# Kernel tuning notes

Measured on AMD Instinct MI355X. Metric: run time of the kernel, lower is better.

The kernel has to match this reference:

```python
import jax, jax.numpy as jnp
import numpy as np

B, C, H, W, K = 4, 96, 56, 56, 9
CM = 2 * C  # graph-conv output channels (standard Grapher: 2*in_channels)


def setup_inputs() -> dict:
    key = jax.random.key(0)
    ks = jax.random.split(key, 6)
    x = jax.random.normal(ks[0], (B, C, H, W), jnp.float32)
    fc1_w = jax.random.normal(ks[1], (C, C), jnp.float32) * 0.05
    fc1_b = jnp.zeros((C,), jnp.float32)
    gconv_w = jax.random.normal(ks[2], (CM, 2 * C), jnp.float32) * 0.05
    gconv_b = jnp.zeros((CM,), jnp.float32)
    fc2_w = jax.random.normal(ks[3], (C, CM), jnp.float32) * 0.05
    fc2_b = jnp.zeros((C,), jnp.float32)
    sa_w = jax.random.normal(ks[4], (1, 2, 7, 7), jnp.float32) * 0.05
    return dict(x=x, fc1_w=fc1_w, fc1_b=fc1_b, gconv_w=gconv_w, gconv_b=gconv_b,
                fc2_w=fc2_w, fc2_b=fc2_b, sa_w=sa_w)


def _knn_idx(xf, k):
    # xf: (B, C, N) -> (B, N, k) nearest-neighbor indices (includes self),
    # matching dense_knn_matrix: topk of negative squared euclidean distance.
    x2 = jnp.sum(xf * xf, axis=1)                       # (B, N)
    inner = jnp.einsum('bcn,bcm->bnm', xf, xf)          # (B, N, N)
    dist = x2[:, :, None] - 2.0 * inner + x2[:, None, :]
    _, idx = jax.lax.top_k(-dist, k)                    # (B, N, k)
    return idx


def _grapher(x, fc1_w, fc1_b, gconv_w, gconv_b, fc2_w, fc2_b, sa_w):
    shortcut = x
    # fc1: 1x1 conv C -> C
    h = jnp.einsum('bchw,oc->bohw', x, fc1_w) + fc1_b[None, :, None, None]
    b, c, hh, ww = h.shape
    n = hh * ww
    xf = h.reshape(b, c, n)                              # nodes: (B, C, N)
    idx = _knn_idx(xf, K)                                # dynamic KNN graph
    # EdgeConv2d: gather x_j at neighbor indices, x_i = center
    xt = jnp.transpose(xf, (0, 2, 1))                    # (B, N, C)
    x_j = jax.vmap(lambda t, i: t[i])(xt, idx)           # (B, N, K, C)
    x_j = jnp.transpose(x_j, (0, 3, 1, 2))               # (B, C, N, K)
    x_i = xf[:, :, :, None]                              # (B, C, N, 1)
    feat = jnp.concatenate(
        [jnp.broadcast_to(x_i, x_j.shape), x_j - x_i], axis=1)  # (B, 2C, N, K)
    e = jnp.einsum('bcnk,oc->bonk', feat, gconv_w) + gconv_b[None, :, None, None]
    e = jax.nn.relu(e)
    g = jnp.max(e, axis=-1)                              # max over K neighbors
    g = g.reshape(b, CM, hh, ww)
    # fc2: 1x1 conv 2C -> C
    out = jnp.einsum('bchw,oc->bohw', g, fc2_w) + fc2_b[None, :, None, None]
    # SpatialAttention: channel mean/max -> 7x7 conv -> sigmoid gate
    avg = jnp.mean(out, axis=1, keepdims=True)
    mx = jnp.max(out, axis=1, keepdims=True)
    sa_in = jnp.concatenate([avg, mx], axis=1)           # (B, 2, H, W)
    att = jax.lax.conv_general_dilated(
        sa_in, sa_w, window_strides=(1, 1), padding=[(3, 3), (3, 3)],
        dimension_numbers=('NCHW', 'OIHW', 'NCHW'))
    att = jax.nn.sigmoid(att)
    return out * att + shortcut


def reference(x, fc1_w, fc1_b, gconv_w, gconv_b, fc2_w, fc2_b, sa_w):
    return _grapher(x, fc1_w, fc1_b, gconv_w, gconv_b, fc2_w, fc2_b, sa_w)
```

## Files before the change

kernel.cpp:

```cpp
#include <hip/hip_runtime.h>

#define BB 4
#define CC 96
#define NN 3136
#define FLTMAX 3.402823466e+38f
#define CAP 44
#define DELTA 1.0f

typedef unsigned short ushort_t;
typedef __attribute__((ext_vector_type(8))) short bf16x8;
typedef __attribute__((ext_vector_type(4))) float f32x4;

__device__ __forceinline__ ushort_t f2bf(float f) {
    unsigned u = __float_as_uint(f);
    unsigned r = (u + 0x7fff + ((u >> 16) & 1)) >> 16;
    return (ushort_t)r;
}
__device__ __forceinline__ float bf2f(ushort_t us) {
    return __uint_as_float(((unsigned)us) << 16);
}


__global__ __launch_bounds__(256) void k_fc1(const float* __restrict__ x, const float* __restrict__ w,
                                             const float* __restrict__ bias, float* __restrict__ h,
                                             float* __restrict__ x2g,
                                             ushort_t* __restrict__ hAhi,
                                             float* __restrict__ hT) {
    __shared__ float sm[96 * 98 + 96 * 64];
    float* wT = sm;
    float* xl = sm + 96 * 98;
    const int tid = threadIdx.x;
    const int n0 = blockIdx.x * 64;
    const int b = blockIdx.y;
    for (int i = tid; i < 96 * 96; i += 256) {
        int o = i / 96, c = i - o * 96;
        wT[c * 98 + o] = w[i];
    }
    const float* xb = x + (size_t)b * CC * NN;
    for (int i = tid; i < 96 * 64; i += 256) {
        int c = i >> 6, nl = i & 63;
        xl[i] = xb[(size_t)c * NN + n0 + nl];
    }
    __syncthreads();
    const int tr = tid >> 4, tc = tid & 15;
    float acc[6][4];
#pragma unroll
    for (int i = 0; i < 6; ++i)
#pragma unroll
        for (int j = 0; j < 4; ++j) acc[i][j] = 0.f;
#pragma unroll 4
    for (int c = 0; c < 96; ++c) {
        float4 xv = *(const float4*)&xl[c * 64 + tc * 4];
        const float* wp = &wT[c * 98 + tr * 6];
        float2 w01 = *(const float2*)(wp);
        float2 w23 = *(const float2*)(wp + 2);
        float2 w45 = *(const float2*)(wp + 4);
        float wv[6] = {w01.x, w01.y, w23.x, w23.y, w45.x, w45.y};
        float xj[4] = {xv.x, xv.y, xv.z, xv.w};
#pragma unroll
        for (int i = 0; i < 6; ++i)
#pragma unroll
            for (int j = 0; j < 4; ++j) acc[i][j] = fmaf(wv[i], xj[j], acc[i][j]);
    }
    float* hb = h + (size_t)b * CC * NN;
    float* hTb = hT + (size_t)b * NN * 96;
    ushort_t* thi = hAhi + (size_t)b * 602112;
#pragma unroll
    for (int i = 0; i < 6; ++i) {
        float bi = bias[tr * 6 + i];
        acc[i][0] += bi; acc[i][1] += bi; acc[i][2] += bi; acc[i][3] += bi;
        float4 o4 = make_float4(acc[i][0], acc[i][1], acc[i][2], acc[i][3]);
        *(float4*)&hb[(size_t)(tr * 6 + i) * NN + n0 + tc * 4] = o4;
        const int c = tr * 6 + i;
        const int cpart = c >> 3;
#pragma unroll
        for (int j = 0; j < 4; ++j) {
            const int n = n0 + tc * 4 + j;
            const int idx = (((n >> 5) * 12 + cpart) * 32 + (n & 31)) * 8 + (c & 7);
            thi[idx] = f2bf(acc[i][j]);
            hTb[(size_t)n * 96 + c] = acc[i][j];
        }
    }
    __syncthreads();
#pragma unroll
    for (int j = 0; j < 4; ++j) {
        float s = 0.f;
#pragma unroll
        for (int i = 0; i < 6; ++i) s = fmaf(acc[i][j], acc[i][j], s);
        sm[tr * 64 + tc * 4 + j] = s;
    }
    __syncthreads();
    if (tid < 64) {
        float s = 0.f;
#pragma unroll
        for (int t = 0; t < 16; ++t) s += sm[t * 64 + tid];
        x2g[(size_t)b * NN + n0 + tid] = s;
    }
}

#define MFMA_TILE_HI(t, acc0, acc1, acc2, acc3)                                       \
    {                                                                                 \
        const int abase_ = (t) * 6144;                                                \
        _Pragma("unroll")                                                             \
        for (int ks_ = 0; ks_ < 3; ++ks_) {                                           \
            const int base_ = abase_ + ks_ * 1024;                                    \
            bf16x8 a0_ = *(const bf16x8*)(hHi + base_ + aoff0);                       \
            bf16x8 a1_ = *(const bf16x8*)(hHi + base_ + aoff1);                       \
            bf16x8 a2_ = *(const bf16x8*)(hHi + base_ + 3072 + aoff0);                \
            bf16x8 a3_ = *(const bf16x8*)(hHi + base_ + 3072 + aoff1);                \
            acc0 = __builtin_amdgcn_mfma_f32_16x16x32_bf16(a0_, bhi[ks_], acc0, 0, 0, 0); \
            acc1 = __builtin_amdgcn_mfma_f32_16x16x32_bf16(a1_, bhi[ks_], acc1, 0, 0, 0); \
            acc2 = __builtin_amdgcn_mfma_f32_16x16x32_bf16(a2_, bhi[ks_], acc2, 0, 0, 0); \
            acc3 = __builtin_amdgcn_mfma_f32_16x16x32_bf16(a3_, bhi[ks_], acc3, 0, 0, 0); \
        }                                                                             \
    }

__global__ __launch_bounds__(256) void k_dist(const ushort_t* __restrict__ hAhi,
                                              const float* __restrict__ x2,
                                              int* __restrict__ cand_cnt,
                                              int* __restrict__ cand_idx) {
    __shared__ float thrb[32][24];
    __shared__ float thr_s[32];
    __shared__ int   cnt[32];
    __shared__ int   list[32][CAP];
    const int tid = threadIdx.x;
    const int nb = blockIdx.x, q = blockIdx.y, b = blockIdx.z;
    const int w = tid >> 6, l = tid & 63;
    const int ln = l & 15, lq = l >> 4;
    const int p = w >> 1;
    const int kl_off = lq * 256;
    const ushort_t* hHi = hAhi + (size_t)b * 602112;
    const float* x2b = x2 + (size_t)b * NN;

    const int lane32n = (w & 1) * 16 + ln;
    bf16x8 bhi[3];
#pragma unroll
    for (int ks = 0; ks < 3; ++ks) {
        const int off = nb * 3072 + ks * 1024 + kl_off + lane32n * 8;
        bhi[ks] = *(const bf16x8*)(hHi + off);
    }
    const int aoff0 = kl_off + ln * 8;
    const int aoff1 = kl_off + (16 + ln) * 8;

    const int qb0 = (q == 0) ? 0 : (q == 1) ? 13 : (q == 2) ? 25 : 37;
    const int qb1 = (q == 0) ? 13 : (q == 1) ? 25 : (q == 2) ? 37 : 49;
    const int tstart = qb0 + p;

    unsigned scache[7][8];
    float lv0 = FLTMAX, lv1 = FLTMAX, lv2 = FLTMAX;
#pragma unroll
    for (int ti = 0; ti < 7; ++ti) {
        const int t = tstart + 2 * ti;
        if (t < qb1) {
            const int m0 = t * 64;
            f32x4 acc0 = {0.f, 0.f, 0.f, 0.f}, acc1 = {0.f, 0.f, 0.f, 0.f};
            f32x4 acc2 = {0.f, 0.f, 0.f, 0.f}, acc3 = {0.f, 0.f, 0.f, 0.f};
            MFMA_TILE_HI(t, acc0, acc1, acc2, acc3);
#pragma unroll
            for (int msub = 0; msub < 4; ++msub) {
                f32x4 a = (msub == 0) ? acc0 : (msub == 1) ? acc1 : (msub == 2) ? acc2 : acc3;
                const int mb = m0 + msub * 16 + lq * 4;
                float4 xv = *(const float4*)&x2b[mb];
                float s0 = fmaf(-2.f, a[0], xv.x);
                float s1 = fmaf(-2.f, a[1], xv.y);
                float s2 = fmaf(-2.f, a[2], xv.z);
                float s3 = fmaf(-2.f, a[3], xv.w);
                scache[ti][msub * 2 + 0] = ((unsigned)f2bf(s0) << 16) | (unsigned)f2bf(s1);
                scache[ti][msub * 2 + 1] = ((unsigned)f2bf(s2) << 16) | (unsigned)f2bf(s3);
                float ss[4] = {s0, s1, s2, s3};
#pragma unroll
                for (int r = 0; r < 4; ++r) {
                    float v = ss[r];
                    float t0 = fminf(lv0, v);
                    lv0 = fmaxf(t0, lv1);
                    float t1 = fminf(t0, lv1);
                    lv1 = fmaxf(t1, lv2);
                    lv2 = fminf(t1, lv2);
                }
            }
        }
    }
    {
        const int sidx = (p * 4 + lq) * 3;
        thrb[lane32n][sidx + 0] = lv0;
        thrb[lane32n][sidx + 1] = lv1;
        thrb[lane32n][sidx + 2] = lv2;
    }
    __syncthreads();
    if (tid < 32) {
        float tmp[24];
#pragma unroll
        for (int j = 0; j < 24; ++j) tmp[j] = thrb[tid][j];
        float last = FLTMAX;
        for (int kk = 0; kk < 9; ++kk) {
            float mn = FLTMAX; int ms = 0;
            for (int j = 0; j < 24; ++j)
                if (tmp[j] < mn) { mn = tmp[j]; ms = j; }
            tmp[ms] = FLTMAX;
            last = mn;
        }
        thr_s[tid] = last + DELTA;
        cnt[tid] = 0;
    }
    __syncthreads();
    const float thr = thr_s[lane32n];

#pragma unroll
    for (int ti = 0; ti < 7; ++ti) {
        const int t = tstart + 2 * ti;
        if (t < qb1) {
            const int m0 = t * 64;
#pragma unroll
            for (int msub = 0; msub < 4; ++msub) {
                const int mb = m0 + msub * 16 + lq * 4;
                const unsigned u01 = scache[ti][msub * 2 + 0];
                const unsigned u23 = scache[ti][msub * 2 + 1];
                float vv[4] = {bf2f((ushort_t)(u01 >> 16)), bf2f((ushort_t)(u01 & 0xffff)),
                               bf2f((ushort_t)(u23 >> 16)), bf2f((ushort_t)(u23 & 0xffff))};
#pragma unroll
                for (int r = 0; r < 4; ++r) {
                    if (vv[r] <= thr) {
                        int pos = atomicAdd(&cnt[lane32n], 1);
                        if (pos < CAP) list[lane32n][pos] = mb + r;
                    }
                }
            }
        }
    }
    __syncthreads();
    const size_t rowbase = (size_t)b * NN + nb * 32;
    if (tid < 32) cand_cnt[(rowbase + tid) * 4 + q] = min(cnt[tid], CAP);
    for (int i = tid; i < 32 * CAP; i += 256) {
        int r = i / CAP, j = i - r * CAP;
        if (j < min(cnt[r], CAP))
            cand_idx[((rowbase + r) * 4 + q) * CAP + j] = list[r][j];
    }
}

__global__ __launch_bounds__(256) void k_merge9(const int* __restrict__ cand_cnt,
                                                const int* __restrict__ cand_idx,
                                                const float* __restrict__ hT,
                                                const float* __restrict__ x2,
                                                int* __restrict__ idx9) {
    const int tid = threadIdx.x;
    const int wv = tid >> 6, lane = tid & 63;
    const size_t n = (size_t)blockIdx.x * 4 + wv;
    const int b = (int)(n / NN);
    const int nn = (int)(n - (size_t)b * NN);
    const int c0 = cand_cnt[n * 4 + 0];
    const int c1 = cand_cnt[n * 4 + 1];
    const int c2 = cand_cnt[n * 4 + 2];
    const int c3 = cand_cnt[n * 4 + 3];
    const int p1 = c0, p2 = c0 + c1, p3 = c0 + c1 + c2;
    const int ct = p3 + c3;
    const float* hTb = hT + (size_t)b * NN * 96;
    const float* own = hTb + (size_t)nn * 96;
    const float* x2b = x2 + (size_t)b * NN;

    float vs[3]; int cjs[3];
#pragma unroll
    for (int t = 0; t < 3; ++t) { vs[t] = FLTMAX; cjs[t] = 0x7fffffff; }
#pragma unroll
    for (int t = 0; t < 3; ++t) {
        const int j = lane + 64 * t;
        if (j < ct) {
            const int qq = (j >= p1) + (j >= p2) + (j >= p3);
            const int base = (qq == 0) ? 0 : (qq == 1) ? p1 : (qq == 2) ? p2 : p3;
            const int cj = cand_idx[(n * 4 + qq) * CAP + (j - base)];
            const float* cr = hTb + (size_t)cj * 96;
            float dot = 0.f;
#pragma unroll
            for (int i = 0; i < 24; ++i) {
                float4 rv = *(const float4*)&own[i * 4];
                float4 cv4 = *(const float4*)&cr[i * 4];
                dot = fmaf(rv.x, cv4.x, dot);
                dot = fmaf(rv.y, cv4.y, dot);
                dot = fmaf(rv.z, cv4.z, dot);
                dot = fmaf(rv.w, cv4.w, dot);
            }
            vs[t] = fmaf(-2.f, dot, x2b[cj]);
            cjs[t] = cj;
        }
    }
    int* dst = idx9 + n * 9;
    for (int kk = 0; kk < 9; ++kk) {
        float mv = vs[0]; int mi = cjs[0];
        if (vs[1] < mv || (vs[1] == mv && cjs[1] < mi)) { mv = vs[1]; mi = cjs[1]; }
        if (vs[2] < mv || (vs[2] == mv && cjs[2] < mi)) { mv = vs[2]; mi = cjs[2]; }
#pragma unroll
        for (int s = 32; s; s >>= 1) {
            float ov = __shfl_xor(mv, s, 64);
            int oi = __shfl_xor(mi, s, 64);
            if (ov < mv || (ov == mv && oi < mi)) { mv = ov; mi = oi; }
        }
        if (lane == 0) dst[kk] = mi;
#pragma unroll
        for (int t = 0; t < 3; ++t)
            if (cjs[t] == mi) vs[t] = FLTMAX;
    }
}

__global__ __launch_bounds__(256) void k_ac(const float* __restrict__ h, const float* __restrict__ gw,
                                            const float* __restrict__ gb, ushort_t* __restrict__ acT) {
    __shared__ float sm[96 * 98 + 96 * 64];
    float* wT = sm;
    float* hl = sm + 96 * 98;
    const int tid = threadIdx.x;
    const int n0 = blockIdx.x * 64, ot = blockIdx.y, b = blockIdx.z;
    for (int i = tid; i < 96 * 96; i += 256) {
        int o = i / 96, c = i - o * 96;
        float v;
        if (ot < 2) {
            const float* gwp = gw + (size_t)(ot * 96 + o) * 192;
            v = gwp[c] - gwp[96 + c];
        } else {
            v = gw[(size_t)((ot - 2) * 96 + o) * 192 + 96 + c];
        }
        wT[c * 98 + o] = v;
    }
    const float* hb = h + (size_t)b * CC * NN;
    for (int i = tid; i < 96 * 64; i += 256) {
        int c = i >> 6, nl = i & 63;
        hl[i] = hb[(size_t)c * NN + n0 + nl];
    }
    __syncthreads();
    const int tr = tid >> 4, tc = tid & 15;
    float acc[6][4];
#pragma unroll
    for (int i = 0; i < 6; ++i)
#pragma unroll
        for (int j = 0; j < 4; ++j) acc[i][j] = 0.f;
#pragma unroll 4
    for (int c = 0; c < 96; ++c) {
        float4 xv = *(const float4*)&hl[c * 64 + tc * 4];
        const float* wp = &wT[c * 98 + tr * 6];
        float2 w01 = *(const float2*)(wp);
        float2 w23 = *(const float2*)(wp + 2);
        float2 w45 = *(const float2*)(wp + 4);
        float wv[6] = {w01.x, w01.y, w23.x, w23.y, w45.x, w45.y};
        float xj[4] = {xv.x, xv.y, xv.z, xv.w};
#pragma unroll
        for (int i = 0; i < 6; ++i)
#pragma unroll
            for (int j = 0; j < 4; ++j) acc[i][j] = fmaf(wv[i], xj[j], acc[i][j]);
    }
    const int obase = ot * 96 + tr * 6;
    float bs[6];
#pragma unroll
    for (int i = 0; i < 6; ++i) bs[i] = (ot < 2) ? gb[obase + i] : 0.f;
#pragma unroll
    for (int j = 0; j < 4; ++j) {
        ushort_t* dst = acT + ((size_t)b * NN + n0 + tc * 4 + j) * 384 + obase;
        ushort2 p0, p1, p2;
        p0.x = f2bf(acc[0][j] + bs[0]); p0.y = f2bf(acc[1][j] + bs[1]);
        p1.x = f2bf(acc[2][j] + bs[2]); p1.y = f2bf(acc[3][j] + bs[3]);
        p2.x = f2bf(acc[4][j] + bs[4]); p2.y = f2bf(acc[5][j] + bs[5]);
        *(ushort2*)(dst + 0) = p0;
        *(ushort2*)(dst + 2) = p1;
        *(ushort2*)(dst + 4) = p2;
    }
}

__global__ __launch_bounds__(256) void k_gather(const ushort_t* __restrict__ acT,
                                                const int* __restrict__ idx9,
                                                float* __restrict__ gT) {
    const int lane = threadIdx.x & 63;
    const int wv = threadIdx.x >> 6;
    const int b = blockIdx.y;
    const int nb = blockIdx.x * 16 + wv * 4;
    for (int r = 0; r < 4; ++r) {
        const int n = nb + r;
        const ushort_t* ar = acT + ((size_t)b * NN + n) * 384;
        float a0 = bf2f(ar[lane]), a1 = bf2f(ar[lane + 64]), a2 = bf2f(ar[lane + 128]);
        const int* ip = idx9 + ((size_t)b * NN + n) * 9;
        int jj[9];
#pragma unroll
        for (int k = 0; k < 9; ++k) jj[k] = ip[k];
        float m0 = -FLTMAX, m1 = -FLTMAX, m2 = -FLTMAX;
#pragma unroll
        for (int k = 0; k < 9; ++k) {
            const ushort_t* cr = acT + ((size_t)b * NN + jj[k]) * 384 + 192;
            m0 = fmaxf(m0, a0 + bf2f(cr[lane]));
            m1 = fmaxf(m1, a1 + bf2f(cr[lane + 64]));
            m2 = fmaxf(m2, a2 + bf2f(cr[lane + 128]));
        }
        float* gr = gT + ((size_t)b * NN + n) * 192;
        gr[lane] = fmaxf(m0, 0.f);
        gr[lane + 64] = fmaxf(m1, 0.f);
        gr[lane + 128] = fmaxf(m2, 0.f);
    }
}

__global__ __launch_bounds__(256) void k_fc2(const float* __restrict__ gT, const float* __restrict__ w,
                                             const float* __restrict__ bias, float* __restrict__ out,
                                             float* __restrict__ sa_in) {
    __shared__ float Wc[96 * 36];
    __shared__ float Gc[64 * 36];
    const int tid = threadIdx.x;
    const int n0 = blockIdx.x * 64, b = blockIdx.y;
    const int tr = tid >> 4, tc = tid & 15;
    float acc[6][4];
#pragma unroll
    for (int i = 0; i < 6; ++i)
#pragma unroll
        for (int j = 0; j < 4; ++j) acc[i][j] = 0.f;
    for (int kc = 0; kc < 192; kc += 32) {
        for (int i = tid; i < 96 * 32; i += 256) {
            int c = i >> 5, k = i & 31;
            Wc[c * 36 + k] = w[(size_t)c * 192 + kc + k];
        }
        for (int i = tid; i < 64 * 32; i += 256) {
            int nl = i >> 5, k = i & 31;
            Gc[nl * 36 + k] = gT[((size_t)b * NN + n0 + nl) * 192 + kc + k];
        }
        __syncthreads();
#pragma unroll
        for (int k = 0; k < 32; k += 4) {
            float4 wv[6]; float4 gv[4];
#pragma unroll
            for (int i = 0; i < 6; ++i) wv[i] = *(const float4*)&Wc[(tr * 6 + i) * 36 + k];
#pragma unroll
            for (int j = 0; j < 4; ++j) gv[j] = *(const float4*)&Gc[(tc * 4 + j) * 36 + k];
#pragma unroll
            for (int i = 0; i < 6; ++i)
#pragma unroll
                for (int j = 0; j < 4; ++j) {
                    acc[i][j] = fmaf(wv[i].x, gv[j].x, acc[i][j]);
                    acc[i][j] = fmaf(wv[i].y, gv[j].y, acc[i][j]);
                    acc[i][j] = fmaf(wv[i].z, gv[j].z, acc[i][j]);
                    acc[i][j] = fmaf(wv[i].w, gv[j].w, acc[i][j]);
                }
        }
        __syncthreads();
    }
    float* ob = out + (size_t)b * CC * NN;
    float bs[6];
#pragma unroll
    for (int i = 0; i < 6; ++i) bs[i] = bias[tr * 6 + i];
    float ps[4], pm[4];
#pragma unroll
    for (int j = 0; j < 4; ++j) { ps[j] = 0.f; pm[j] = -FLTMAX; }
#pragma unroll
    for (int i = 0; i < 6; ++i) {
        float o0 = acc[i][0] + bs[i], o1 = acc[i][1] + bs[i];
        float o2 = acc[i][2] + bs[i], o3 = acc[i][3] + bs[i];
        *(float4*)&ob[(size_t)(tr * 6 + i) * NN + n0 + tc * 4] = make_float4(o0, o1, o2, o3);
        ps[0] += o0; ps[1] += o1; ps[2] += o2; ps[3] += o3;
        pm[0] = fmaxf(pm[0], o0); pm[1] = fmaxf(pm[1], o1);
        pm[2] = fmaxf(pm[2], o2); pm[3] = fmaxf(pm[3], o3);
    }
    float* red  = Wc;
    float* red2 = Wc + 1024;
#pragma unroll
    for (int j = 0; j < 4; ++j) {
        red[tr * 64 + tc * 4 + j]  = ps[j];
        red2[tr * 64 + tc * 4 + j] = pm[j];
    }
    __syncthreads();
    if (tid < 64) {
        float s_ = 0.f, m_ = -FLTMAX;
#pragma unroll
        for (int t = 0; t < 16; ++t) { s_ += red[t * 64 + tid]; m_ = fmaxf(m_, red2[t * 64 + tid]); }
        sa_in[(size_t)b * 2 * NN + n0 + tid] = s_ * (1.0f / 96.0f);
        sa_in[(size_t)b * 2 * NN + NN + n0 + tid] = m_;
    }
}

__global__ __launch_bounds__(256) void k_att(const float* __restrict__ sa_in, const float* __restrict__ sw,
                                             const float* __restrict__ x, float* __restrict__ out) {
    int n = blockIdx.x * 256 + threadIdx.x;
    int b = blockIdx.y;
    if (n >= NN) return;
    int y = n / 56, xw = n - y * 56;
    float acc = 0.f;
#pragma unroll
    for (int ci = 0; ci < 2; ++ci) {
        const float* sb = sa_in + ((size_t)b * 2 + ci) * NN;
#pragma unroll
        for (int dy = 0; dy < 7; ++dy) {
            int yy = y + dy - 3;
            if ((unsigned)yy < 56u) {
#pragma unroll
                for (int dx = 0; dx < 7; ++dx) {
                    int xx = xw + dx - 3;
                    if ((unsigned)xx < 56u)
                        acc = fmaf(sb[yy * 56 + xx], sw[(ci * 7 + dy) * 7 + dx], acc);
                }
            }
        }
    }
    float att = 1.f / (1.f + expf(-acc));
    const float* xb = x + (size_t)b * CC * NN + n;
    float* ob = out + (size_t)b * CC * NN + n;
#pragma unroll 4
    for (int c = 0; c < 96; ++c) {
        size_t o = (size_t)c * NN;
        ob[o] = fmaf(ob[o], att, xb[o]);
    }
}

extern "C" void kernel_launch(void* const* d_in, const int* in_sizes, int n_in,
                              void* d_out, int out_size, void* d_ws, size_t ws_size,
                              hipStream_t stream) {
    (void)in_sizes; (void)n_in; (void)out_size; (void)ws_size;
    const float* x       = (const float*)d_in[0];
    const float* fc1_w   = (const float*)d_in[1];
    const float* fc1_b   = (const float*)d_in[2];
    const float* gconv_w = (const float*)d_in[3];
    const float* gconv_b = (const float*)d_in[4];
    const float* fc2_w   = (const float*)d_in[5];
    const float* fc2_b   = (const float*)d_in[6];
    const float* sa_w    = (const float*)d_in[7];
    float* out = (float*)d_out;

    float* ws   = (float*)d_ws;
    float* h    = ws;
    float* x2   = h + (size_t)BB * CC * NN;
    int*   idx9 = (int*)(x2 + BB * NN);
    float* regA = (float*)(idx9 + (size_t)BB * NN * 9);
    ushort_t* hAhi = (ushort_t*)regA;
    ushort_t* acT  = (ushort_t*)regA;
    float* hT   = regA + 2408448;
    float* regB = hT + 1204224;
    int*   cand_idx = (int*)regB;
    int*   cand_cnt = (int*)(regB + 2207744);
    float* gT   = regB;
    float* sa_in = regB + 2408448;

    k_fc1   <<<dim3(49, BB), 256, 0, stream>>>(x, fc1_w, fc1_b, h, x2, hAhi, hT);
    k_dist  <<<dim3(98, 4, BB), 256, 0, stream>>>(hAhi, x2, cand_cnt, cand_idx);
    k_merge9<<<dim3(3136), 256, 0, stream>>>(cand_cnt, cand_idx, hT, x2, idx9);
    k_ac    <<<dim3(49, 4, BB), 256, 0, stream>>>(h, gconv_w, gconv_b, acT);
    k_gather<<<dim3(196, BB), 256, 0, stream>>>(acT, idx9, gT);
    k_fc2   <<<dim3(49, BB), 256, 0, stream>>>(gT, fc2_w, fc2_b, out, sa_in);
    k_att   <<<dim3(13, BB), 256, 0, stream>>>(sa_in, sa_w, x, out);
}
```

Before: 269.9 us.

## Prefilter KNN candidates by packed approximate distance; shrink fc2 tile for more blocks

The distance kernel now stores each candidate's bf16 approximate distance in the upper 16 bits of its index word. The merge kernel uses these packed values to find the 9th-smallest approximate distance. It then recomputes exact fp32 dot products only for candidates within a fixed margin of that value, which skips most of the 96-wide gathers. Separately, fc2 drops from a 64-node tile to a 16-node tile with one output column per thread, launching four times as many blocks to fill more CUs, at the cost of reloading the weight tile more often. The margin-based pruning assumes the bf16 error is bounded by the margin and could change the selected neighbours if it is not.

```diff
diff --git a/kernel.cpp b/kernel.cpp
--- a/kernel.cpp
+++ b/kernel.cpp
@@ -6,6 +6,7 @@
 #define FLTMAX 3.402823466e+38f
 #define CAP 44
 #define DELTA 1.0f
+#define PREF_MARGIN 0.8f
 
 typedef unsigned short ushort_t;
 typedef __attribute__((ext_vector_type(8))) short bf16x8;
@@ -215,13 +216,12 @@
                 const int mb = m0 + msub * 16 + lq * 4;
                 const unsigned u01 = scache[ti][msub * 2 + 0];
                 const unsigned u23 = scache[ti][msub * 2 + 1];
-                float vv[4] = {bf2f((ushort_t)(u01 >> 16)), bf2f((ushort_t)(u01 & 0xffff)),
-                               bf2f((ushort_t)(u23 >> 16)), bf2f((ushort_t)(u23 & 0xffff))};
+                unsigned bits[4] = {u01 >> 16, u01 & 0xffffu, u23 >> 16, u23 & 0xffffu};
 #pragma unroll
                 for (int r = 0; r < 4; ++r) {
-                    if (vv[r] <= thr) {
+                    if (bf2f((ushort_t)bits[r]) <= thr) {
                         int pos = atomicAdd(&cnt[lane32n], 1);
-                        if (pos < CAP) list[lane32n][pos] = mb + r;
+                        if (pos < CAP) list[lane32n][pos] = (int)((bits[r] << 16) | (unsigned)(mb + r));
                     }
                 }
             }
@@ -257,16 +257,46 @@
     const float* own = hTb + (size_t)nn * 96;
     const float* x2b = x2 + (size_t)b * NN;
 
-    float vs[3]; int cjs[3];
-#pragma unroll
-    for (int t = 0; t < 3; ++t) { vs[t] = FLTMAX; cjs[t] = 0x7fffffff; }
+    float av[3]; int cjs[3];
+#pragma unroll
+    for (int t = 0; t < 3; ++t) { av[t] = FLTMAX; cjs[t] = 0x7fffffff; }
 #pragma unroll
     for (int t = 0; t < 3; ++t) {
         const int j = lane + 64 * t;
         if (j < ct) {
             const int qq = (j >= p1) + (j >= p2) + (j >= p3);
             const int base = (qq == 0) ? 0 : (qq == 1) ? p1 : (qq == 2) ? p2 : p3;
-            const int cj = cand_idx[(n * 4 + qq) * CAP + (j - base)];
+            const unsigned u = (unsigned)cand_idx[(n * 4 + qq) * CAP + (j - base)];
+            av[t] = bf2f((ushort_t)(u >> 16));
+            cjs[t] = (int)(u & 0xffffu);
+        }
+    }
+    float a9 = FLTMAX;
+    {
+        float tv[3] = {av[0], av[1], av[2]};
+        for (int kk = 0; kk < 9; ++kk) {
+            float mv = tv[0]; int ms = 0;
+            if (tv[1] < mv) { mv = tv[1]; ms = 1; }
+            if (tv[2] < mv) { mv = tv[2]; ms = 2; }
+            int mid = lane * 4 + ms;
+#pragma unroll
+            for (int s = 32; s; s >>= 1) {
+                float ov = __shfl_xor(mv, s, 64);
+                int oi = __shfl_xor(mid, s, 64);
+                if (ov < mv || (ov == mv && oi < mid)) { mv = ov; mid = oi; }
+            }
+            a9 = mv;
+            if ((mid >> 2) == lane) tv[mid & 3] = FLTMAX;
+        }
+    }
+    const float cutoff = a9 + PREF_MARGIN;
+
+    float vs[3];
+#pragma unroll
+    for (int t = 0; t < 3; ++t) {
+        vs[t] = FLTMAX;
+        if (av[t] <= cutoff) {
+            const int cj = cjs[t];
             const float* cr = hTb + (size_t)cj * 96;
             float dot = 0.f;
 #pragma unroll
@@ -279,7 +309,6 @@
                 dot = fmaf(rv.w, cv4.w, dot);
             }
             vs[t] = fmaf(-2.f, dot, x2b[cj]);
-            cjs[t] = cj;
         }
     }
     int* dst = idx9 + n * 9;
@@ -395,72 +424,54 @@
                                              const float* __restrict__ bias, float* __restrict__ out,
                                              float* __restrict__ sa_in) {
     __shared__ float Wc[96 * 36];
-    __shared__ float Gc[64 * 36];
+    __shared__ float Gc[16 * 36];
+    __shared__ float red[2][16][17];
     const int tid = threadIdx.x;
-    const int n0 = blockIdx.x * 64, b = blockIdx.y;
+    const int n0 = blockIdx.x * 16, b = blockIdx.y;
     const int tr = tid >> 4, tc = tid & 15;
-    float acc[6][4];
-#pragma unroll
-    for (int i = 0; i < 6; ++i)
-#pragma unroll
-        for (int j = 0; j < 4; ++j) acc[i][j] = 0.f;
+    float acc[6];
+#pragma unroll
+    for (int i = 0; i < 6; ++i) acc[i] = 0.f;
     for (int kc = 0; kc < 192; kc += 32) {
         for (int i = tid; i < 96 * 32; i += 256) {
             int c = i >> 5, k = i & 31;
             Wc[c * 36 + k] = w[(size_t)c * 192 + kc + k];
         }
-        for (int i = tid; i < 64 * 32; i += 256) {
+        for (int i = tid; i < 16 * 32; i += 256) {
             int nl = i >> 5, k = i & 31;
             Gc[nl * 36 + k] = gT[((size_t)b * NN + n0 + nl) * 192 + kc + k];
         }
         __syncthreads();
 #pragma unroll
         for (int k = 0; k < 32; k += 4) {
-            float4 wv[6]; float4 gv[4];
-#pragma unroll
-            for (int i = 0; i < 6; ++i) wv[i] = *(const float4*)&Wc[(tr * 6 + i) * 36 + k];
-#pragma unroll
-            for (int j = 0; j < 4; ++j) gv[j] = *(const float4*)&Gc[(tc * 4 + j) * 36 + k];
-#pragma unroll
-            for (int i = 0; i < 6; ++i)
-#pragma unroll
-                for (int j = 0; j < 4; ++j) {
-                    acc[i][j] = fmaf(wv[i].x, gv[j].x, acc[i][j]);
-                    acc[i][j] = fmaf(wv[i].y, gv[j].y, acc[i][j]);
-                    acc[i][j] = fmaf(wv[i].z, gv[j].z, acc[i][j]);
-                    acc[i][j] = fmaf(wv[i].w, gv[j].w, acc[i][j]);
-                }
+            float4 gv = *(const float4*)&Gc[tc * 36 + k];
+#pragma unroll
+            for (int i = 0; i < 6; ++i) {
+                float4 wv = *(const float4*)&Wc[(tr * 6 + i) * 36 + k];
+                acc[i] = fmaf(wv.x, gv.x, acc[i]);
+                acc[i] = fmaf(wv.y, gv.y, acc[i]);
+                acc[i] = fmaf(wv.z, gv.z, acc[i]);
+                acc[i] = fmaf(wv.w, gv.w, acc[i]);
+            }
         }
         __syncthreads();
     }
     float* ob = out + (size_t)b * CC * NN;
-    float bs[6];
-#pragma unroll
-    for (int i = 0; i < 6; ++i) bs[i] = bias[tr * 6 + i];
-    float ps[4], pm[4];
-#pragma unroll
-    for (int j = 0; j < 4; ++j) { ps[j] = 0.f; pm[j] = -FLTMAX; }
+    float ps = 0.f, pm = -FLTMAX;
 #pragma unroll
     for (int i = 0; i < 6; ++i) {
-        float o0 = acc[i][0] + bs[i], o1 = acc[i][1] + bs[i];
-        float o2 = acc[i][2] + bs[i], o3 = acc[i][3] + bs[i];
-        *(float4*)&ob[(size_t)(tr * 6 + i) * NN + n0 + tc * 4] = make_float4(o0, o1, o2, o3);
-        ps[0] += o0; ps[1] += o1; ps[2] += o2; ps[3] += o3;
-        pm[0] = fmaxf(pm[0], o0); pm[1] = fmaxf(pm[1], o1);
-        pm[2] = fmaxf(pm[2], o2); pm[3] = fmaxf(pm[3], o3);
-    }
-    float* red  = Wc;
-    float* red2 = Wc + 1024;
-#pragma unroll
-    for (int j = 0; j < 4; ++j) {
-        red[tr * 64 + tc * 4 + j]  = ps[j];
-        red2[tr * 64 + tc * 4 + j] = pm[j];
-    }
-    __syncthreads();
-    if (tid < 64) {
+        float o = acc[i] + bias[tr * 6 + i];
+        ob[(size_t)(tr * 6 + i) * NN + n0 + tc] = o;
+        ps += o;
+        pm = fmaxf(pm, o);
+    }
+    red[0][tr][tc] = ps;
+    red[1][tr][tc] = pm;
+    __syncthreads();
+    if (tid < 16) {
         float s_ = 0.f, m_ = -FLTMAX;
 #pragma unroll
-        for (int t = 0; t < 16; ++t) { s_ += red[t * 64 + tid]; m_ = fmaxf(m_, red2[t * 64 + tid]); }
+        for (int t = 0; t < 16; ++t) { s_ += red[0][t][tid]; m_ = fmaxf(m_, red[1][t][tid]); }
         sa_in[(size_t)b * 2 * NN + n0 + tid] = s_ * (1.0f / 96.0f);
         sa_in[(size_t)b * 2 * NN + NN + n0 + tid] = m_;
     }
@@ -532,6 +543,6 @@
     k_merge9<<<dim3(3136), 256, 0, stream>>>(cand_cnt, cand_idx, hT, x2, idx9);
     k_ac    <<<dim3(49, 4, BB), 256, 0, stream>>>(h, gconv_w, gconv_b, acT);
     k_gather<<<dim3(196, BB), 256, 0, stream>>>(acT, idx9, gT);
-    k_fc2   <<<dim3(49, BB), 256, 0, stream>>>(gT, fc2_w, fc2_b, out, sa_in);
+    k_fc2   <<<dim3(196, BB), 256, 0, stream>>>(gT, fc2_w, fc2_b, out, sa_in);
     k_att   <<<dim3(13, BB), 256, 0, stream>>>(sa_in, sa_w, x, out);
 }
```

Result: faster. 250.7 us (-7.1%).
